# Optimization experiments

Hardware: AMD Instinct MI355X
Metric: run time of the kernel (lower is better)

The kernel has to match this reference:

```python
import jax, jax.numpy as jnp
import numpy as np

B, S, HID = 2, 2048, 2048
H, KV, D = 16, 8, 128          # query heads, kv heads, head_dim
EPS = 1e-6
THETA = 1000000.0


def setup_inputs() -> dict:
    key = jax.random.key(0)
    ks = jax.random.split(key, 8)
    sc = 0.02
    hidden_states = jax.random.normal(ks[0], (B, S, HID), dtype=jnp.float32)
    Wq = jax.random.normal(ks[1], (HID, H * D), dtype=jnp.float32) * sc
    Wk = jax.random.normal(ks[2], (HID, KV * D), dtype=jnp.float32) * sc
    Wv = jax.random.normal(ks[3], (HID, KV * D), dtype=jnp.float32) * sc
    Wo = jax.random.normal(ks[4], (H * D, HID), dtype=jnp.float32) * sc
    q_norm_w = jnp.ones((D,), dtype=jnp.float32)
    k_norm_w = jnp.ones((D,), dtype=jnp.float32)
    positions = jnp.arange(S, dtype=jnp.int32)
    # causal mask: True = masked (j > i)
    attention_mask = jnp.triu(jnp.ones((S, S), dtype=bool), k=1)
    return {
        "hidden_states": hidden_states, "Wq": Wq, "Wk": Wk, "Wv": Wv,
        "Wo": Wo, "q_norm_w": q_norm_w, "k_norm_w": k_norm_w,
        "positions": positions, "attention_mask": attention_mask,
    }


def _rms_norm(x, w):
    # x: [..., D]; RMSNorm over last dim
    var = jnp.mean(x * x, axis=-1, keepdims=True)
    return x * jax.lax.rsqrt(var + EPS) * w


def _rope(x, positions):
    # x: [B, h, S, D]; standard rotate-half RoPE
    inv_freq = 1.0 / (THETA ** (jnp.arange(0, D, 2, dtype=jnp.float32) / D))
    ang = positions.astype(jnp.float32)[:, None] * inv_freq[None, :]  # [S, D/2]
    cos = jnp.concatenate([jnp.cos(ang), jnp.cos(ang)], axis=-1)      # [S, D]
    sin = jnp.concatenate([jnp.sin(ang), jnp.sin(ang)], axis=-1)
    x1, x2 = x[..., : D // 2], x[..., D // 2:]
    rot = jnp.concatenate([-x2, x1], axis=-1)
    return x * cos + rot * sin


def reference(hidden_states, Wq, Wk, Wv, Wo, q_norm_w, k_norm_w,
              positions, attention_mask):
    b, s, _ = hidden_states.shape
    q = (hidden_states @ Wq).reshape(b, s, H, D).transpose(0, 2, 1, 3)   # [B,H,S,D]
    k = (hidden_states @ Wk).reshape(b, s, KV, D).transpose(0, 2, 1, 3)  # [B,KV,S,D]
    v = (hidden_states @ Wv).reshape(b, s, KV, D).transpose(0, 2, 1, 3)
    q = _rms_norm(q, q_norm_w)
    k = _rms_norm(k, k_norm_w)
    q = _rope(q, positions)
    k = _rope(k, positions)
    # GQA: repeat kv heads
    g = H // KV
    k = jnp.repeat(k, g, axis=1)  # [B,H,S,D]
    v = jnp.repeat(v, g, axis=1)
    scale = 1.0 / np.sqrt(D).astype(np.float32)
    scores = jnp.einsum('bhqd,bhkd->bhqk', q, k) * scale
    scores = jnp.where(attention_mask[None, None, :, :], -jnp.inf, scores)
    attn = jax.nn.softmax(scores, axis=-1)
    out = jnp.einsum('bhqk,bhkd->bhqd', attn, v)
    out = out.transpose(0, 2, 1, 3).reshape(b, s, H * D)
    return out @ Wo
```

## Files before the change

kernel.cpp:

```cpp
#include <hip/hip_runtime.h>
#include <hip/hip_bf16.h>

typedef __hip_bfloat16 bf16;
typedef __attribute__((ext_vector_type(8))) short short8v;
typedef __attribute__((ext_vector_type(4))) float f32x4;

constexpr int nB = 2;
constexpr int nS = 2048;
constexpr int nHID = 2048;
constexpr int nH = 16;
constexpr int nKV = 8;
constexpr int nD = 128;
constexpr int QS = 4096;
constexpr float kEps = 1e-6f;
constexpr float kScale = 0.08838834764831845f;

template <int N>
struct IC {
  static constexpr int value = N;
};

__device__ inline float b2f(unsigned short u) {
  return __uint_as_float(((unsigned)u) << 16);
}
__device__ inline float bf2f(bf16 v) { return __bfloat162float(v); }
__device__ inline short f2bs(float f) {
  bf16 h = __float2bfloat16(f);
  return *reinterpret_cast<short*>(&h);
}
__device__ inline unsigned pack2bf(float a, float b) {
  return ((unsigned)(unsigned short)f2bs(b) << 16) |
         (unsigned)(unsigned short)f2bs(a);
}

__device__ inline void gload_lds16(const bf16* g, bf16* l) {
  __builtin_amdgcn_global_load_lds(
      (const __attribute__((address_space(1))) void*)g,
      (__attribute__((address_space(3))) void*)l, 16, 0, 0);
}

template <int N>
__device__ inline void vwait() {
  asm volatile("s_waitcnt vmcnt(%0)" ::"n"(N) : "memory");
}

__global__ __launch_bounds__(256) void cvt_f32_bf16(
    const float* __restrict__ src, bf16* __restrict__ dst, int n) {
  const int i = (blockIdx.x * 256 + threadIdx.x) * 4;
  if (i >= n) return;
  const float4 v = *reinterpret_cast<const float4*>(src + i);
  ushort4 o;
  o.x = (unsigned short)f2bs(v.x);
  o.y = (unsigned short)f2bs(v.y);
  o.z = (unsigned short)f2bs(v.z);
  o.w = (unsigned short)f2bs(v.w);
  *reinterpret_cast<ushort4*>(dst + i) = o;
}

__global__ __launch_bounds__(256) void transpose_f32_bf16(
    const float* __restrict__ src, bf16* __restrict__ dst, int K, int N) {
  __shared__ float t[32][33];
  const int k0 = blockIdx.y * 32, n0 = blockIdx.x * 32;
  const int c = threadIdx.x & 31, r8 = threadIdx.x >> 5;
#pragma unroll
  for (int i = 0; i < 4; ++i)
    t[r8 + i * 8][c] = src[(size_t)(k0 + r8 + i * 8) * N + n0 + c];
  __syncthreads();
#pragma unroll
  for (int i = 0; i < 4; ++i)
    dst[(size_t)(n0 + r8 + i * 8) * K + k0 + c] =
        __float2bfloat16(t[c][r8 + i * 8]);
}

template <int BM, typename OUT_T>
__global__ __launch_bounds__(512) void gemm_8ph(
    const bf16* __restrict__ A, const bf16* __restrict__ Bt,
    OUT_T* __restrict__ C, int M, int N, int K) {
  constexpr int LA = BM / 128;
  constexpr int LB = 2;
  constexpr int MF = BM / 32;
  constexpr int MFH = MF / 2;
  constexpr int W = 2 * (LA + LB);
  constexpr int LDSB = 2 * BM * 32 + 2 * 256 * 32;
  __shared__ bf16 lds[2 * LDSB];

  const int tid = threadIdx.x;
  const int wave = tid >> 6, lane = tid & 63;
  const int lr = lane & 15, lg = lane >> 4;
  const int wm = wave >> 2, wn = wave & 3;
  const int m0 = blockIdx.y * BM, n0 = blockIdx.x * 256;
  const int srow = tid >> 2, scol = (tid & 3) * 8;

  auto stageA = [&](int t, int kk) {
    bf16* dst = lds + (t & 1) * LDSB + kk * (BM * 32) + wave * 512;
    const bf16* src = A + (size_t)(m0 + srow) * K + t * 64 + kk * 32 + scol;
#pragma unroll
    for (int j = 0; j < LA; ++j)
      gload_lds16(src + (size_t)(j * 128) * K, dst + j * 4096);
  };
  auto stageB = [&](int t, int kk) {
    bf16* dst =
        lds + (t & 1) * LDSB + 2 * BM * 32 + kk * (256 * 32) + wave * 512;
    const bf16* src = Bt + (size_t)(n0 + srow) * K + t * 64 + kk * 32 + scol;
#pragma unroll
    for (int j = 0; j < LB; ++j)
      gload_lds16(src + (size_t)(j * 128) * K, dst + j * 4096);
  };

  f32x4 acc[MF][4];
#pragma unroll
  for (int m = 0; m < MF; ++m)
#pragma unroll
    for (int n = 0; n < 4; ++n) acc[m][n] = (f32x4){0.f, 0.f, 0.f, 0.f};
  short8v bfr[4];

  auto phase = [&](auto WC, int buf, int kk, int mh, auto stageFn) {
    constexpr int WAIT = decltype(WC)::value;
    if constexpr (WAIT >= 0) vwait<WAIT>();
    __builtin_amdgcn_s_barrier();
    asm volatile("" ::: "memory");
    if (mh == 0) {
      const bf16* bb = lds + buf * LDSB + 2 * BM * 32 + kk * (256 * 32);
#pragma unroll
      for (int ni = 0; ni < 4; ++ni)
        bfr[ni] = *reinterpret_cast<const short8v*>(
            bb + (wn * 64 + ni * 16 + lr) * 32 + lg * 8);
    }
    short8v af[MFH];
    const bf16* ab = lds + buf * LDSB + kk * (BM * 32);
#pragma unroll
    for (int ii = 0; ii < MFH; ++ii)
      af[ii] = *reinterpret_cast<const short8v*>(
          ab + (wm * (BM / 2) + (mh * MFH + ii) * 16 + lr) * 32 + lg * 8);
    stageFn();
    asm volatile("s_waitcnt lgkmcnt(0)" ::: "memory");
    __builtin_amdgcn_sched_barrier(0);
    __builtin_amdgcn_s_setprio(1);
#pragma unroll
    for (int ii = 0; ii < MFH; ++ii)
#pragma unroll
      for (int ni = 0; ni < 4; ++ni)
        acc[mh * MFH + ii][ni] = __builtin_amdgcn_mfma_f32_16x16x32_bf16(
            af[ii], bfr[ni], acc[mh * MFH + ii][ni], 0, 0, 0);
    __builtin_amdgcn_s_setprio(0);
  };

  const int NT = K / 64;
  stageA(0, 0);
  stageB(0, 0);
  stageA(0, 1);
  stageB(0, 1);
  stageA(1, 0);
  stageB(1, 0);

  for (int t = 0; t < NT - 1; ++t) {
    const int buf = t & 1;
    phase(IC<W>{}, buf, 0, 0, [&] { stageA(t + 1, 1); });
    phase(IC<-1>{}, buf, 0, 1, [&] { stageB(t + 1, 1); });
    phase(IC<W>{}, buf, 1, 0, [&] {
      if (t < NT - 2) stageA(t + 2, 0);
    });
    phase(IC<-1>{}, buf, 1, 1, [&] {
      if (t < NT - 2) stageB(t + 2, 0);
    });
  }
  {
    const int buf = (NT - 1) & 1;
    phase(IC<LA + LB>{}, buf, 0, 0, [&] {});
    phase(IC<-1>{}, buf, 0, 1, [&] {});
    phase(IC<0>{}, buf, 1, 0, [&] {});
    phase(IC<-1>{}, buf, 1, 1, [&] {});
  }

#pragma unroll
  for (int m = 0; m < MF; ++m)
#pragma unroll
    for (int n = 0; n < 4; ++n)
#pragma unroll
      for (int r = 0; r < 4; ++r) {
        const int row = m0 + wm * (BM / 2) + m * 16 + 4 * lg + r;
        const int col = n0 + wn * 64 + n * 16 + lr;
        if constexpr (sizeof(OUT_T) == 2)
          C[(size_t)row * N + col] = __float2bfloat16(acc[m][n][r]);
        else
          C[(size_t)row * N + col] = acc[m][n][r];
      }
}

__global__ __launch_bounds__(128) void norm_rope_fused(
    bf16* __restrict__ qkv, const float* __restrict__ qw,
    const float* __restrict__ kw) {
  const int row = blockIdx.x;
  const int head = blockIdx.y;
  const int t = threadIdx.x;
  const int s = row & (nS - 1);
  const bool isQ = head < nH;
  const int col = isQ ? head * nD : 2048 + (head - nH) * nD;
  const float* w = isQ ? qw : kw;
  bf16* xp = qkv + (size_t)row * QS + col;
  const float v = bf2f(xp[t]);
  float ss = v * v;
#pragma unroll
  for (int off = 32; off > 0; off >>= 1) ss += __shfl_xor(ss, off);
  __shared__ float wsum[2];
  __shared__ float buf[nD];
  if ((t & 63) == 0) wsum[t >> 6] = ss;
  __syncthreads();
  const float inv = rsqrtf((wsum[0] + wsum[1]) * (1.0f / nD) + kEps);
  const float nv = v * inv * w[t];
  buf[t] = nv;
  __syncthreads();
  const float partner = buf[t ^ 64];
  const float rot = (t < 64) ? -partner : partner;
  const int j = t & 63;
  const float invf = expf(-(float)j * (13.815510557964274f / 64.0f));
  const float ang = (float)s * invf;
  const float outv = nv * cosf(ang) + rot * sinf(ang);
  xp[t] = __float2bfloat16(outv);
}

constexpr int BQ = 128, BKT = 64;

__global__ __launch_bounds__(512) void attn_mfma(
    const bf16* __restrict__ QKV, bf16* __restrict__ O) {
  const int l = blockIdx.x;
  const int bh = l & 31;
  const int rr0 = l >> 5;
  const int qb = (rr0 < 8) ? 15 - rr0 : rr0 - 8;
  const int b = bh >> 4, h = bh & 15, kvh = h >> 1;
  const int q0 = qb * BQ;
  const int nt = 2 * qb + 2;
  const int tid = threadIdx.x;
  const int wave = tid >> 6, lane = tid & 63;
  const int lr = lane & 15, lg = lane >> 4;

  __shared__ bf16 Ks[BKT][136];
  __shared__ bf16 Vt[nD][72];
  __shared__ bf16 Pl[8 * 1024];

  const bf16* Qbase = QKV + (size_t)b * nS * QS + h * nD;
  const bf16* Kbase = QKV + (size_t)b * nS * QS + 2048 + kvh * nD;
  const bf16* Vbase = QKV + (size_t)b * nS * QS + 3072 + kvh * nD;

  const int krow = tid >> 3, kcc = (tid & 7) * 16;
  const int vkey = tid & 63, vdc = (tid >> 6) * 16;

  short8v kreg[2], vreg[2];
  auto gload = [&](int kt) {
    const bf16* ksrc = Kbase + (size_t)(kt + krow) * QS + kcc;
    const bf16* vsrc = Vbase + (size_t)(kt + vkey) * QS + vdc;
    kreg[0] = *reinterpret_cast<const short8v*>(ksrc);
    kreg[1] = *reinterpret_cast<const short8v*>(ksrc + 8);
    vreg[0] = *reinterpret_cast<const short8v*>(vsrc);
    vreg[1] = *reinterpret_cast<const short8v*>(vsrc + 8);
  };
  auto lwrite = [&]() {
    *reinterpret_cast<short8v*>(&Ks[krow][kcc]) = kreg[0];
    *reinterpret_cast<short8v*>(&Ks[krow][kcc + 8]) = kreg[1];
#pragma unroll
    for (int i = 0; i < 2; ++i)
#pragma unroll
      for (int j = 0; j < 8; ++j)
        *reinterpret_cast<short*>(&Vt[vdc + 8 * i + j][vkey]) = vreg[i][j];
  };

  short8v qf[4];
  {
    const bf16* qrow = Qbase + (size_t)(q0 + 16 * wave + lr) * QS;
#pragma unroll
    for (int dc = 0; dc < 4; ++dc)
      qf[dc] = *reinterpret_cast<const short8v*>(qrow + 32 * dc + 8 * lg);
  }

  f32x4 of[8];
#pragma unroll
  for (int n = 0; n < 8; ++n) of[n] = (f32x4){0.f, 0.f, 0.f, 0.f};
  float m_run = -1e30f, l_run = 0.f;

  const int plbase = (wave << 10) + (lr << 6);
  const int plswz = (lr & 7) << 3;

  gload(0);
  lwrite();
  __syncthreads();

  for (int j = 0; j < nt; ++j) {
    const int kt = j * BKT;
    const bool have_next = (j + 1 < nt);
    if (have_next) gload((j + 1) * BKT);

    f32x4 s[4];
    __builtin_amdgcn_s_setprio(1);
#pragma unroll
    for (int sub = 0; sub < 4; ++sub) {
      f32x4 acc = {0.f, 0.f, 0.f, 0.f};
#pragma unroll
      for (int dc = 0; dc < 4; ++dc) {
        const short8v kf = *reinterpret_cast<const short8v*>(
            &Ks[16 * sub + lr][32 * dc + 8 * lg]);
        acc = __builtin_amdgcn_mfma_f32_16x16x32_bf16(kf, qf[dc], acc, 0, 0, 0);
      }
      s[sub] = acc;
    }
    __builtin_amdgcn_s_setprio(0);

    const bool needMask = (kt + BKT > q0 + 16 * wave);
#pragma unroll
    for (int sub = 0; sub < 4; ++sub)
#pragma unroll
      for (int r = 0; r < 4; ++r) {
        float v = s[sub][r] * kScale;
        if (needMask && (kt + 16 * sub + 4 * lg + r > q0 + 16 * wave + lr))
          v = -1e30f;
        s[sub][r] = v;
      }

    float pmax = -1e30f;
#pragma unroll
    for (int sub = 0; sub < 4; ++sub)
#pragma unroll
      for (int r = 0; r < 4; ++r) pmax = fmaxf(pmax, s[sub][r]);
    pmax = fmaxf(pmax, __shfl_xor(pmax, 16));
    pmax = fmaxf(pmax, __shfl_xor(pmax, 32));

    if (!__all(pmax - m_run <= 8.f)) {
      const float mt = fmaxf(m_run, pmax);
      const float corr = __expf(m_run - mt);
#pragma unroll
      for (int n = 0; n < 8; ++n) of[n] *= corr;
      l_run *= corr;
      m_run = mt;
    }

    float p[4][4];
    float lsum = 0.f;
#pragma unroll
    for (int sub = 0; sub < 4; ++sub)
#pragma unroll
      for (int r = 0; r < 4; ++r) {
        const float e = __expf(s[sub][r] - m_run);
        p[sub][r] = e;
        lsum += e;
      }
    lsum += __shfl_xor(lsum, 16);
    lsum += __shfl_xor(lsum, 32);
    l_run += lsum;

#pragma unroll
    for (int sub = 0; sub < 4; ++sub)
#pragma unroll
      for (int rp = 0; rp < 2; ++rp) {
        const int col = 16 * sub + 4 * lg + 2 * rp;
        *reinterpret_cast<unsigned*>(&Pl[plbase + (col ^ plswz)]) =
            pack2bf(p[sub][2 * rp], p[sub][2 * rp + 1]);
      }

    __builtin_amdgcn_s_setprio(1);
#pragma unroll
    for (int kk = 0; kk < 2; ++kk) {
      const short8v pb = *reinterpret_cast<const short8v*>(
          &Pl[plbase + ((32 * kk + 8 * lg) ^ plswz)]);
#pragma unroll
      for (int n = 0; n < 8; ++n) {
        const short8v vf = *reinterpret_cast<const short8v*>(
            &Vt[16 * n + lr][32 * kk + 8 * lg]);
        of[n] = __builtin_amdgcn_mfma_f32_16x16x32_bf16(vf, pb, of[n], 0, 0, 0);
      }
    }
    __builtin_amdgcn_s_setprio(0);

    if (have_next) {
      __syncthreads();
      lwrite();
      __syncthreads();
    }
  }

  {
    const float inv = 1.0f / l_run;
    bf16* orow = O + ((size_t)(b * nS + q0 + 16 * wave + lr)) * (nH * nD) +
                 h * nD + 4 * lg;
#pragma unroll
    for (int n = 0; n < 8; ++n)
#pragma unroll
      for (int rp = 0; rp < 2; ++rp)
        *reinterpret_cast<unsigned*>(orow + 16 * n + 2 * rp) =
            pack2bf(of[n][2 * rp] * inv, of[n][2 * rp + 1] * inv);
  }
}

extern "C" void kernel_launch(void* const* d_in, const int* in_sizes, int n_in,
                              void* d_out, int out_size, void* d_ws,
                              size_t ws_size, hipStream_t stream) {
  const float* hs = (const float*)d_in[0];
  const float* Wq = (const float*)d_in[1];
  const float* Wk = (const float*)d_in[2];
  const float* Wv = (const float*)d_in[3];
  const float* Wo = (const float*)d_in[4];
  const float* qw = (const float*)d_in[5];
  const float* kw = (const float*)d_in[6];

  const int M = nB * nS;
  char* ws = (char*)d_ws;
  size_t off = 0;
  auto alloc = [&](size_t bytes) {
    char* p = ws + off;
    off += bytes;
    return p;
  };
  bf16* hsb = (bf16*)alloc((size_t)M * nHID * 2);
  bf16* att = hsb;
  bf16* qkv = (bf16*)alloc((size_t)M * QS * 2);
  bf16* Wcat = (bf16*)alloc((size_t)QS * nHID * 2);
  bf16* Wot = (bf16*)alloc((size_t)nH * nD * nHID * 2);
  float* out = (float*)d_out;

  const int nHsElems = M * nHID;
  cvt_f32_bf16<<<(nHsElems / 4 + 255) / 256, 256, 0, stream>>>(hs, hsb,
                                                               nHsElems);
  transpose_f32_bf16<<<dim3(nH * nD / 32, nHID / 32), 256, 0, stream>>>(
      Wq, Wcat, nHID, nH * nD);
  transpose_f32_bf16<<<dim3(nKV * nD / 32, nHID / 32), 256, 0, stream>>>(
      Wk, Wcat + (size_t)2048 * nHID, nHID, nKV * nD);
  transpose_f32_bf16<<<dim3(nKV * nD / 32, nHID / 32), 256, 0, stream>>>(
      Wv, Wcat + (size_t)3072 * nHID, nHID, nKV * nD);
  transpose_f32_bf16<<<dim3(nHID / 32, nH * nD / 32), 256, 0, stream>>>(
      Wo, Wot, nH * nD, nHID);

  gemm_8ph<256, bf16><<<dim3(QS / 256, M / 256), 512, 0, stream>>>(
      hsb, Wcat, qkv, M, QS, nHID);

  norm_rope_fused<<<dim3(M, nH + nKV), 128, 0, stream>>>(qkv, qw, kw);

  attn_mfma<<<dim3(512), 512, 0, stream>>>(qkv, att);

  gemm_8ph<128, float><<<dim3(nHID / 256, M / 128), 512, 0, stream>>>(
      att, Wot, out, M, nHID, nH * nD);
}
```

Before: 260.1 us.

## Process two 16-row query fragments per wave in attention with 256-thread blocks

The attention kernel now uses 4 waves of 256 threads instead of 8 waves, with each wave handling 32 query rows as two MFMA fragments. Each K and V fragment read from LDS is therefore reused for two query tiles. The change also vectorizes the V transpose stores into a swizzled Vt layout, and it skips MFMAs for fragments that lie entirely above the causal diagonal. In exchange each wave needs more registers, and fewer waves per block are available to hide latency.

```diff
diff --git a/kernel.cpp b/kernel.cpp
--- a/kernel.cpp
+++ b/kernel.cpp
@@ -221,7 +221,7 @@
 
 constexpr int BQ = 128, BKT = 64;
 
-__global__ __launch_bounds__(512) void attn_mfma(
+__global__ __launch_bounds__(256) void attn_mfma(
     const bf16* __restrict__ QKV, bf16* __restrict__ O) {
   const int l = blockIdx.x;
   const int bh = l & 31;
@@ -236,48 +236,60 @@
 
   __shared__ bf16 Ks[BKT][136];
   __shared__ bf16 Vt[nD][72];
-  __shared__ bf16 Pl[8 * 1024];
+  __shared__ bf16 Pl[4 * 2048];
 
   const bf16* Qbase = QKV + (size_t)b * nS * QS + h * nD;
   const bf16* Kbase = QKV + (size_t)b * nS * QS + 2048 + kvh * nD;
   const bf16* Vbase = QKV + (size_t)b * nS * QS + 3072 + kvh * nD;
 
-  const int krow = tid >> 3, kcc = (tid & 7) * 16;
-  const int vkey = tid & 63, vdc = (tid >> 6) * 16;
-
-  short8v kreg[2], vreg[2];
+  const int kr = tid >> 2, kc = (tid & 3) * 32;
+  const int vk = (tid & 15) * 4, vd = (tid >> 4) * 8;
+
+  short8v kreg[4], vreg[4];
   auto gload = [&](int kt) {
-    const bf16* ksrc = Kbase + (size_t)(kt + krow) * QS + kcc;
-    const bf16* vsrc = Vbase + (size_t)(kt + vkey) * QS + vdc;
-    kreg[0] = *reinterpret_cast<const short8v*>(ksrc);
-    kreg[1] = *reinterpret_cast<const short8v*>(ksrc + 8);
-    vreg[0] = *reinterpret_cast<const short8v*>(vsrc);
-    vreg[1] = *reinterpret_cast<const short8v*>(vsrc + 8);
+    const bf16* ksrc = Kbase + (size_t)(kt + kr) * QS + kc;
+#pragma unroll
+    for (int i = 0; i < 4; ++i)
+      kreg[i] = *reinterpret_cast<const short8v*>(ksrc + 8 * i);
+    const bf16* vsrc = Vbase + (size_t)(kt + vk) * QS + vd;
+#pragma unroll
+    for (int i = 0; i < 4; ++i)
+      vreg[i] = *reinterpret_cast<const short8v*>(vsrc + (size_t)i * QS);
   };
   auto lwrite = [&]() {
-    *reinterpret_cast<short8v*>(&Ks[krow][kcc]) = kreg[0];
-    *reinterpret_cast<short8v*>(&Ks[krow][kcc + 8]) = kreg[1];
-#pragma unroll
-    for (int i = 0; i < 2; ++i)
-#pragma unroll
-      for (int j = 0; j < 8; ++j)
-        *reinterpret_cast<short*>(&Vt[vdc + 8 * i + j][vkey]) = vreg[i][j];
-  };
-
-  short8v qf[4];
-  {
-    const bf16* qrow = Qbase + (size_t)(q0 + 16 * wave + lr) * QS;
+#pragma unroll
+    for (int i = 0; i < 4; ++i)
+      *reinterpret_cast<short8v*>(&Ks[kr][kc + 8 * i]) = kreg[i];
+#pragma unroll
+    for (int j = 0; j < 8; ++j) {
+      const int dd = vd + j;
+      const int kcol = vk ^ ((((dd) >> 3) & 3) << 3);
+      ushort4 pk;
+      pk.x = (unsigned short)vreg[0][j];
+      pk.y = (unsigned short)vreg[1][j];
+      pk.z = (unsigned short)vreg[2][j];
+      pk.w = (unsigned short)vreg[3][j];
+      *reinterpret_cast<ushort4*>(&Vt[dd][kcol]) = pk;
+    }
+  };
+
+  short8v qf[2][4];
+#pragma unroll
+  for (int f = 0; f < 2; ++f) {
+    const bf16* qrow = Qbase + (size_t)(q0 + 32 * wave + 16 * f + lr) * QS;
 #pragma unroll
     for (int dc = 0; dc < 4; ++dc)
-      qf[dc] = *reinterpret_cast<const short8v*>(qrow + 32 * dc + 8 * lg);
+      qf[f][dc] = *reinterpret_cast<const short8v*>(qrow + 32 * dc + 8 * lg);
   }
 
-  f32x4 of[8];
-#pragma unroll
-  for (int n = 0; n < 8; ++n) of[n] = (f32x4){0.f, 0.f, 0.f, 0.f};
-  float m_run = -1e30f, l_run = 0.f;
-
-  const int plbase = (wave << 10) + (lr << 6);
+  f32x4 of[2][8];
+#pragma unroll
+  for (int f = 0; f < 2; ++f)
+#pragma unroll
+    for (int n = 0; n < 8; ++n) of[f][n] = (f32x4){0.f, 0.f, 0.f, 0.f};
+  float m_run[2] = {-1e30f, -1e30f}, l_run[2] = {0.f, 0.f};
+
+  const int plw = wave * 2048;
   const int plswz = (lr & 7) << 3;
 
   gload(0);
@@ -289,82 +301,97 @@
     const bool have_next = (j + 1 < nt);
     if (have_next) gload((j + 1) * BKT);
 
-    f32x4 s[4];
+    const bool act[2] = {kt <= q0 + 32 * wave + 15, kt <= q0 + 32 * wave + 31};
+
+    f32x4 s[2][4];
     __builtin_amdgcn_s_setprio(1);
 #pragma unroll
     for (int sub = 0; sub < 4; ++sub) {
-      f32x4 acc = {0.f, 0.f, 0.f, 0.f};
+      f32x4 a0 = {0.f, 0.f, 0.f, 0.f}, a1 = {0.f, 0.f, 0.f, 0.f};
 #pragma unroll
       for (int dc = 0; dc < 4; ++dc) {
         const short8v kf = *reinterpret_cast<const short8v*>(
             &Ks[16 * sub + lr][32 * dc + 8 * lg]);
-        acc = __builtin_amdgcn_mfma_f32_16x16x32_bf16(kf, qf[dc], acc, 0, 0, 0);
+        if (act[0])
+          a0 = __builtin_amdgcn_mfma_f32_16x16x32_bf16(kf, qf[0][dc], a0, 0, 0,
+                                                       0);
+        if (act[1])
+          a1 = __builtin_amdgcn_mfma_f32_16x16x32_bf16(kf, qf[1][dc], a1, 0, 0,
+                                                       0);
       }
-      s[sub] = acc;
+      s[0][sub] = a0;
+      s[1][sub] = a1;
     }
     __builtin_amdgcn_s_setprio(0);
 
-    const bool needMask = (kt + BKT > q0 + 16 * wave);
-#pragma unroll
-    for (int sub = 0; sub < 4; ++sub)
-#pragma unroll
-      for (int r = 0; r < 4; ++r) {
-        float v = s[sub][r] * kScale;
-        if (needMask && (kt + 16 * sub + 4 * lg + r > q0 + 16 * wave + lr))
-          v = -1e30f;
-        s[sub][r] = v;
+#pragma unroll
+    for (int f = 0; f < 2; ++f) {
+      if (!act[f]) continue;
+      const int qcol = q0 + 32 * wave + 16 * f + lr;
+      const bool needMask = (kt + BKT > q0 + 32 * wave + 16 * f);
+#pragma unroll
+      for (int sub = 0; sub < 4; ++sub)
+#pragma unroll
+        for (int r = 0; r < 4; ++r) {
+          float v = s[f][sub][r] * kScale;
+          if (needMask && (kt + 16 * sub + 4 * lg + r > qcol)) v = -1e30f;
+          s[f][sub][r] = v;
+        }
+      float pmax = -1e30f;
+#pragma unroll
+      for (int sub = 0; sub < 4; ++sub)
+#pragma unroll
+        for (int r = 0; r < 4; ++r) pmax = fmaxf(pmax, s[f][sub][r]);
+      pmax = fmaxf(pmax, __shfl_xor(pmax, 16));
+      pmax = fmaxf(pmax, __shfl_xor(pmax, 32));
+
+      if (!__all(pmax - m_run[f] <= 8.f)) {
+        const float mt = fmaxf(m_run[f], pmax);
+        const float corr = __expf(m_run[f] - mt);
+#pragma unroll
+        for (int n = 0; n < 8; ++n) of[f][n] *= corr;
+        l_run[f] *= corr;
+        m_run[f] = mt;
       }
 
-    float pmax = -1e30f;
-#pragma unroll
-    for (int sub = 0; sub < 4; ++sub)
-#pragma unroll
-      for (int r = 0; r < 4; ++r) pmax = fmaxf(pmax, s[sub][r]);
-    pmax = fmaxf(pmax, __shfl_xor(pmax, 16));
-    pmax = fmaxf(pmax, __shfl_xor(pmax, 32));
-
-    if (!__all(pmax - m_run <= 8.f)) {
-      const float mt = fmaxf(m_run, pmax);
-      const float corr = __expf(m_run - mt);
-#pragma unroll
-      for (int n = 0; n < 8; ++n) of[n] *= corr;
-      l_run *= corr;
-      m_run = mt;
-    }
-
-    float p[4][4];
-    float lsum = 0.f;
-#pragma unroll
-    for (int sub = 0; sub < 4; ++sub)
-#pragma unroll
-      for (int r = 0; r < 4; ++r) {
-        const float e = __expf(s[sub][r] - m_run);
-        p[sub][r] = e;
-        lsum += e;
+      float lsum = 0.f;
+#pragma unroll
+      for (int sub = 0; sub < 4; ++sub) {
+        float e0 = __expf(s[f][sub][0] - m_run[f]);
+        float e1 = __expf(s[f][sub][1] - m_run[f]);
+        float e2 = __expf(s[f][sub][2] - m_run[f]);
+        float e3 = __expf(s[f][sub][3] - m_run[f]);
+        lsum += (e0 + e1) + (e2 + e3);
+        const int col0 = (16 * sub + 4 * lg) ^ plswz;
+        *reinterpret_cast<unsigned*>(&Pl[plw + (16 * f + lr) * 64 + col0]) =
+            pack2bf(e0, e1);
+        *reinterpret_cast<unsigned*>(
+            &Pl[plw + (16 * f + lr) * 64 + col0 + 2]) = pack2bf(e2, e3);
       }
-    lsum += __shfl_xor(lsum, 16);
-    lsum += __shfl_xor(lsum, 32);
-    l_run += lsum;
-
-#pragma unroll
-    for (int sub = 0; sub < 4; ++sub)
-#pragma unroll
-      for (int rp = 0; rp < 2; ++rp) {
-        const int col = 16 * sub + 4 * lg + 2 * rp;
-        *reinterpret_cast<unsigned*>(&Pl[plbase + (col ^ plswz)]) =
-            pack2bf(p[sub][2 * rp], p[sub][2 * rp + 1]);
-      }
+      lsum += __shfl_xor(lsum, 16);
+      lsum += __shfl_xor(lsum, 32);
+      l_run[f] += lsum;
+    }
 
     __builtin_amdgcn_s_setprio(1);
 #pragma unroll
     for (int kk = 0; kk < 2; ++kk) {
-      const short8v pb = *reinterpret_cast<const short8v*>(
-          &Pl[plbase + ((32 * kk + 8 * lg) ^ plswz)]);
+      const int pcol = (32 * kk + 8 * lg) ^ plswz;
+      const short8v pb0 =
+          *reinterpret_cast<const short8v*>(&Pl[plw + lr * 64 + pcol]);
+      const short8v pb1 =
+          *reinterpret_cast<const short8v*>(&Pl[plw + (16 + lr) * 64 + pcol]);
 #pragma unroll
       for (int n = 0; n < 8; ++n) {
-        const short8v vf = *reinterpret_cast<const short8v*>(
-            &Vt[16 * n + lr][32 * kk + 8 * lg]);
-        of[n] = __builtin_amdgcn_mfma_f32_16x16x32_bf16(vf, pb, of[n], 0, 0, 0);
+        const int d = 16 * n + lr;
+        const int vcol = (32 * kk + 8 * lg) ^ ((((d) >> 3) & 3) << 3);
+        const short8v vf = *reinterpret_cast<const short8v*>(&Vt[d][vcol]);
+        if (act[0])
+          of[0][n] =
+              __builtin_amdgcn_mfma_f32_16x16x32_bf16(vf, pb0, of[0][n], 0, 0, 0);
+        if (act[1])
+          of[1][n] =
+              __builtin_amdgcn_mfma_f32_16x16x32_bf16(vf, pb1, of[1][n], 0, 0, 0);
       }
     }
     __builtin_amdgcn_s_setprio(0);
@@ -376,16 +403,18 @@
     }
   }
 
-  {
-    const float inv = 1.0f / l_run;
-    bf16* orow = O + ((size_t)(b * nS + q0 + 16 * wave + lr)) * (nH * nD) +
-                 h * nD + 4 * lg;
+#pragma unroll
+  for (int f = 0; f < 2; ++f) {
+    const float inv = 1.0f / l_run[f];
+    bf16* orow =
+        O + ((size_t)(b * nS + q0 + 32 * wave + 16 * f + lr)) * (nH * nD) +
+        h * nD + 4 * lg;
 #pragma unroll
     for (int n = 0; n < 8; ++n)
 #pragma unroll
       for (int rp = 0; rp < 2; ++rp)
         *reinterpret_cast<unsigned*>(orow + 16 * n + 2 * rp) =
-            pack2bf(of[n][2 * rp] * inv, of[n][2 * rp + 1] * inv);
+            pack2bf(of[f][n][2 * rp] * inv, of[f][n][2 * rp + 1] * inv);
   }
 }
 
@@ -432,7 +461,7 @@
 
   norm_rope_fused<<<dim3(M, nH + nKV), 128, 0, stream>>>(qkv, qw, kw);
 
-  attn_mfma<<<dim3(512), 512, 0, stream>>>(qkv, att);
+  attn_mfma<<<dim3(512), 256, 0, stream>>>(qkv, att);
 
   gemm_8ph<128, float><<<dim3(nHID / 256, M / 128), 512, 0, stream>>>(
       att, Wot, out, M, nHID, nH * nD);
```

After: 340.2 us. +30.8%, slower.
